# Kernel tuning notes

Measured on AMD Instinct MI355X. Metric: run time of the kernel, lower is better.

## Reference

```python
import math
import jax, jax.numpy as jnp
import numpy as np

HEADS = 8
D = 128            # model_dim
PE = D // 2        # position_embedding_size (query_positional_score=True)
MAXP = 32          # max_position_embeddings
LN_EPS = 1e-5


def setup_inputs() -> dict:
    key = jax.random.key(0)
    ks = jax.random.split(key, 7)
    bs, h, w = 8, 32, 32
    hidden_state = jax.random.normal(ks[0], (bs, h, w, D), dtype=jnp.float32)
    row_emb = jax.random.normal(ks[1], (2 * MAXP - 1, PE), dtype=jnp.float32) * 0.02
    col_emb = jax.random.normal(ks[2], (2 * MAXP - 1, PE), dtype=jnp.float32) * 0.02
    # torch Linear weights are (out_features, in_features)
    Wq = jax.random.normal(ks[3], (HEADS * D, D), dtype=jnp.float32) / math.sqrt(D)
    Wk = jax.random.normal(ks[4], (HEADS * D, D), dtype=jnp.float32) / math.sqrt(D)
    Wv = jax.random.normal(ks[5], (D, HEADS * D), dtype=jnp.float32) / math.sqrt(HEADS * D)
    bv = jnp.zeros((D,), dtype=jnp.float32)
    ln_g = jnp.ones((D,), dtype=jnp.float32)
    ln_b = jnp.zeros((D,), dtype=jnp.float32)
    return {"hidden_state": hidden_state, "row_emb": row_emb, "col_emb": col_emb,
            "Wq": Wq, "Wk": Wk, "Wv": Wv, "bv": bv, "ln_g": ln_g, "ln_b": ln_b}


def _layer_norm(x, g, b):
    mu = jnp.mean(x, axis=-1, keepdims=True)
    var = jnp.var(x, axis=-1, keepdims=True)
    return (x - mu) * jax.lax.rsqrt(var + LN_EPS) * g + b


def _forward(hidden_state, row_emb, col_emb, Wq, Wk, Wv, bv, ln_g, ln_b):
    bs, h, w, _ = hidden_state.shape
    x = _layer_norm(hidden_state, ln_g, ln_b)  # pre_norm=True
    sqrt_norm = math.sqrt(D)

    # relative indices (static, h == w == 32 here)
    deltas = np.arange(MAXP)[None, :] - np.arange(MAXP)[:, None]
    rel = deltas + MAXP - 1
    row_embeds = row_emb[rel[:w, :w]]  # (w, w, PE)
    col_embeds = col_emb[rel[:h, :h]]  # (h, h, PE)

    # projections; original does .view(bs, w, h, heads, D) on a (bs,h,w,heads*D) tensor
    q = jnp.einsum('bhwc,oc->bhwo', x, Wq).reshape(bs, w, h, HEADS, D)
    k = jnp.einsum('bhwc,oc->bhwo', x, Wk).reshape(bs, w, h, HEADS, D)

    q_row = q[..., :PE]
    q_col = q[..., PE:]
    row_scores = jnp.einsum('bijhd,ikd->bijhk', q_row, row_embeds)
    col_scores = jnp.einsum('bijhd,jld->bijhl', q_col, col_embeds)
    scores = (row_scores[..., :, None] + col_scores[..., None, :]) / sqrt_norm  # bijhkl
    scores = scores.transpose(0, 2, 1, 3, 5, 4)

    content = jnp.einsum('bijhd,bklhd->bijhkl', q, k) / sqrt_norm
    scores = scores + content.transpose(0, 2, 1, 3, 5, 4)  # (bs, h, w, heads, h, w)

    attn_shape = scores.shape
    probs = jax.nn.softmax(scores.reshape(*attn_shape[:-2], -1), axis=-1).reshape(attn_shape)

    # dropout omitted (inference / p=0)
    context = jnp.einsum('bijhkl,bkld->bijhd', probs, x)
    context = context.reshape(bs, h, w, HEADS * D)
    output = jnp.einsum('bhwc,oc->bhwo', context, Wv) + bv + x
    return output, probs


def reference(hidden_state, row_emb, col_emb, Wq, Wk, Wv, bv, ln_g, ln_b):
    return _forward(hidden_state, row_emb, col_emb, Wq, Wk, Wv, bv, ln_g, ln_b)
```

## Files before the change

kernel.cpp:

```cpp
#include <hip/hip_runtime.h>
#include <hip/hip_bf16.h>

#define HEADS 8
#define D 128
#define QSCALE 0.12751743f

typedef unsigned short u16;
typedef unsigned int u32;
typedef __attribute__((ext_vector_type(8))) short short8;
typedef __attribute__((ext_vector_type(4))) float f32x4;

static __device__ inline float sbf2f(short s) {
    return __uint_as_float(((u32)(unsigned short)s) << 16);
}
static __device__ inline u16 f2bf(float f) {
    u32 u = __float_as_uint(f);
    return (u16)((u + 0x7FFFu + ((u >> 16) & 1u)) >> 16);
}
static __device__ inline u32 pk2bf(float a, float b) {
    return (u32)f2bf(a) | ((u32)f2bf(b) << 16);
}
static __device__ inline u32 cvtpk(float a, float b) {
    union { __hip_bfloat162 h; u32 u; } x;
    x.h = __float22bfloat162_rn(make_float2(a, b));
    return x.u;
}
static __device__ inline f32x4 mfma16(short8 a, short8 b, f32x4 c) {
    return __builtin_amdgcn_mfma_f32_16x16x32_bf16(a, b, c, 0, 0, 0);
}
static __device__ inline short8 cvt8(const float* e) {
    f32x4 v0 = *(const f32x4*)e;
    f32x4 v1 = *(const f32x4*)(e + 4);
    union { uint4 u; short8 s; } x;
    x.u = make_uint4(pk2bf(v0[0], v0[1]), pk2bf(v0[2], v0[3]),
                     pk2bf(v1[0], v1[1]), pk2bf(v1[2], v1[3]));
    return x.s;
}
static __device__ __forceinline__ void gload_lds16(const void* g, void* l) {
    __builtin_amdgcn_global_load_lds(
        (const __attribute__((address_space(1))) u32*)g,
        (__attribute__((address_space(3))) u32*)(u32)(uintptr_t)l,
        16, 0, 0);
}

__global__ __launch_bounds__(256) void k_init(const float* __restrict__ hs,
    const float* __restrict__ g, const float* __restrict__ bb,
    const float* __restrict__ Wq, const float* __restrict__ Wk,
    const float* __restrict__ Wv,
    float* __restrict__ xf, u16* __restrict__ xbf, u16* __restrict__ xt,
    u16* __restrict__ wqk, u16* __restrict__ wv)
{
    __shared__ __align__(16) u16 tl[128][136];
    int bid = blockIdx.x;
    int tid = threadIdx.x;
    if (bid < 384) {
        int idx = (bid * 256 + tid) * 4;
        const float* src;
        u16* dst;
        if (idx < 131072)      { src = Wq + idx;            dst = wqk + idx; }
        else if (idx < 262144) { src = Wk + (idx - 131072); dst = wqk + idx; }
        else                   { src = Wv + (idx - 262144); dst = wv + (idx - 262144); }
        f32x4 v = *(const f32x4*)src;
        *(uint2*)dst = make_uint2(pk2bf(v[0], v[1]), pk2bf(v[2], v[3]));
        return;
    }
    int blk = bid - 384;
    int b = blk >> 3, ch = blk & 7;
    int c4 = (tid & 31) * 4;
    f32x4 g4 = *(const f32x4*)(g + c4);
    f32x4 b4 = *(const f32x4*)(bb + c4);
    const float* src = hs + ((size_t)b * 1024 + ch * 128) * 128;
    #pragma unroll
    for (int it = 0; it < 16; ++it) {
        int p = (tid >> 5) + it * 8;
        f32x4 v = *(const f32x4*)(src + (size_t)p * 128 + c4);
        float s1 = (v[0] + v[1]) + (v[2] + v[3]);
        float s2 = (v[0] * v[0] + v[1] * v[1]) + (v[2] * v[2] + v[3] * v[3]);
        #pragma unroll
        for (int off = 1; off < 32; off <<= 1) {
            s1 += __shfl_xor(s1, off);
            s2 += __shfl_xor(s2, off);
        }
        float mu  = s1 * 0.0078125f;
        float var = s2 * 0.0078125f - mu * mu;
        float inv = rsqrtf(var + 1e-5f);
        f32x4 o;
        #pragma unroll
        for (int q = 0; q < 4; ++q) o[q] = (v[q] - mu) * inv * g4[q] + b4[q];
        size_t row = (size_t)b * 1024 + ch * 128 + p;
        *(f32x4*)(xf + row * 128 + c4) = o;
        *(uint2*)(xbf + row * 128 + c4) = make_uint2(pk2bf(o[0], o[1]), pk2bf(o[2], o[3]));
        tl[c4 + 0][p] = f2bf(o[0]);
        tl[c4 + 1][p] = f2bf(o[1]);
        tl[c4 + 2][p] = f2bf(o[2]);
        tl[c4 + 3][p] = f2bf(o[3]);
    }
    __syncthreads();
    u16* dst = xt + (size_t)b * 131072 + ch * 128;
    #pragma unroll
    for (int i = 0; i < 8; ++i) {
        int d = (tid >> 4) + i * 16, c8 = (tid & 15) * 8;
        *(uint4*)(dst + (size_t)d * 1024 + c8) = *(const uint4*)&tl[d][c8];
    }
}

__global__ __launch_bounds__(256) void k_proj(const u16* __restrict__ xbf,
    const u16* __restrict__ wqk,
    u16* __restrict__ q_bf, u16* __restrict__ kt_bf)
{
    int tid = threadIdx.x;
    int w = tid >> 6, l = tid & 63, h = l >> 4, ln = l & 15;
    int t0 = blockIdx.x * 64 + w * 16;
    int o0 = blockIdx.y * 64;
    short8 tb[4];
    #pragma unroll
    for (int s = 0; s < 4; ++s)
        tb[s] = *(const short8*)(xbf + (size_t)(t0 + ln) * 128 + s * 32 + h * 8);
    f32x4 acc[4];
    #pragma unroll
    for (int n = 0; n < 4; ++n) acc[n] = f32x4{0.f, 0.f, 0.f, 0.f};
    #pragma unroll
    for (int n = 0; n < 4; ++n) {
        const u16* wsrc = wqk + (size_t)(o0 + n * 16 + ln) * 128;
        #pragma unroll
        for (int s = 0; s < 4; ++s) {
            short8 wf = *(const short8*)(wsrc + s * 32 + h * 8);
            acc[n] = mfma16(wf, tb[s], acc[n]);
        }
    }
    bool isq = (o0 < 1024);
    float os = isq ? QSCALE : 1.0f;
    int head = (o0 & 1023) >> 7;
    int od = (o0 & 127);
    u16* basep = isq ? q_bf : kt_bf;
    int t = t0 + ln;
    int b = t >> 10, pos = t & 1023;
    size_t row;
    if (isq) row = (size_t)(b * 8 + head) * 1024 + pos;
    else { int I = pos >> 5, J = pos & 31; row = (size_t)(b * 8 + head) * 1024 + (J * 32 + I); }
    u16* dst = basep + row * 128 + od + h * 4;
    #pragma unroll
    for (int n = 0; n < 4; ++n) {
        *(uint2*)(dst + n * 16) = make_uint2(
            pk2bf(acc[n][0] * os, acc[n][1] * os),
            pk2bf(acc[n][2] * os, acc[n][3] * os));
    }
}

__global__ __launch_bounds__(256) void k_bias(const u16* __restrict__ q_bf,
    const float* __restrict__ row_emb, const float* __restrict__ col_emb,
    float* __restrict__ rbias, float* __restrict__ cbias)
{
    __shared__ __align__(16) float cbf[32][68];
    int tid = threadIdx.x;
    int w = tid >> 6, l = tid & 63, h = l >> 4, ln = l & 15;
    int blk = blockIdx.x;
    int bh = blk >> 5, I = blk & 31;
    const u16* qb = q_bf + ((size_t)bh * 1024 + I * 32) * 128;
    size_t obase = (size_t)blk * 1024;
    if (w < 2) {
        short8 a0 = *(const short8*)(qb + (size_t)(w * 16 + ln) * 128 + h * 8);
        short8 a1 = *(const short8*)(qb + (size_t)(w * 16 + ln) * 128 + 32 + h * 8);
        f32x4 o[2] = {f32x4{0,0,0,0}, f32x4{0,0,0,0}};
        #pragma unroll
        for (int n = 0; n < 2; ++n) {
            int K = n * 16 + ln;
            const float* e = row_emb + (size_t)(K - I + 31) * 64 + h * 8;
            o[n] = mfma16(a0, cvt8(e), o[n]);
            o[n] = mfma16(a1, cvt8(e + 32), o[n]);
        }
        #pragma unroll
        for (int n = 0; n < 2; ++n)
            #pragma unroll
            for (int r = 0; r < 4; ++r)
                rbias[obase + (size_t)(w * 16 + h * 4 + r) * 32 + n * 16 + ln] = o[n][r];
    } else {
        int m = w - 2;
        short8 a0 = *(const short8*)(qb + (size_t)(m * 16 + ln) * 128 + 64 + h * 8);
        short8 a1 = *(const short8*)(qb + (size_t)(m * 16 + ln) * 128 + 96 + h * 8);
        f32x4 o[4] = {f32x4{0,0,0,0}, f32x4{0,0,0,0}, f32x4{0,0,0,0}, f32x4{0,0,0,0}};
        #pragma unroll
        for (int n = 0; n < 4; ++n) {
            int p = n * 16 + ln;
            if (p > 62) p = 62;
            const float* e = col_emb + (size_t)p * 64 + h * 8;
            o[n] = mfma16(a0, cvt8(e), o[n]);
            o[n] = mfma16(a1, cvt8(e + 32), o[n]);
        }
        #pragma unroll
        for (int n = 0; n < 4; ++n)
            #pragma unroll
            for (int r = 0; r < 4; ++r)
                cbf[m * 16 + h * 4 + r][n * 16 + ln] = o[n][r];
    }
    __syncthreads();
    int J = tid >> 3, L0 = (tid & 7) * 4;
    float4 g;
    g.x = cbf[J][L0 + 0 - J + 31];
    g.y = cbf[J][L0 + 1 - J + 31];
    g.z = cbf[J][L0 + 2 - J + 31];
    g.w = cbf[J][L0 + 3 - J + 31];
    *(float4*)(cbias + obase + (size_t)J * 32 + L0) = g;
}

__global__ __launch_bounds__(512, 4) void k_attn(const u16* __restrict__ q_bf,
    const u16* __restrict__ kt_bf, const u16* __restrict__ xt_bf,
    const float* __restrict__ rbias, const float* __restrict__ cbias,
    float* __restrict__ probs, u16* __restrict__ ctx_bf)
{
    __shared__ __align__(16) char KT[8 * 8192];
    __shared__ float wred[256];

    int tid = threadIdx.x;
    int w = tid >> 6, l = tid & 63, h = l >> 4, ln = l & 15;
    int flat = blockIdx.x;
    int bh = flat >> 5, I = flat & 31;
    int b = bh >> 3, head = bh & 7;
    int kk0 = w * 128;
    char* reg = KT + w * 8192;
    const char* ktg = (const char*)(kt_bf + ((size_t)bh * 1024 + kk0) * 128);
    int d0 = w * 16;
    const u16* xb = xt_bf + (size_t)b * 131072 + (size_t)(d0 + ln) * 1024 + h * 8;

    const float* rbase = rbias + (size_t)(bh * 32 + I) * 1024;
    const float* cbase = cbias + (size_t)(bh * 32 + I) * 1024;
    f32x4 rbr[2][2], cbr[2];
    #pragma unroll
    for (int n = 0; n < 2; ++n) {
        int J = n * 16 + ln;
        rbr[n][0] = *(const f32x4*)(rbase + J * 32 + h * 4);
        rbr[n][1] = *(const f32x4*)(rbase + J * 32 + 16 + h * 4);
        cbr[n]    = *(const f32x4*)(cbase + J * 32 + w * 4);
    }
    const u16* qbase = q_bf + ((size_t)bh * 1024 + I * 32) * 128;
    short8 q0[4], q1[4];
    #pragma unroll
    for (int s = 0; s < 4; ++s) {
        q0[s] = *(const short8*)(qbase + (size_t)ln * 128 + s * 32 + h * 8);
        q1[s] = *(const short8*)(qbase + (size_t)(16 + ln) * 128 + s * 32 + h * 8);
    }

    auto stage_chunk = [&](int c, int buf) {
        const char* gs = ktg + c * 4096;
        char* ld = reg + buf * 4096;
        #pragma unroll
        for (int i = 0; i < 4; ++i) {
            int key = ((i * 4 + (l >> 4)) & 7) << 4;
            int o = i * 1024 + l * 16;
            gload_lds16(gs + (o ^ key), ld + i * 1024);
        }
    };
    stage_chunk(0, 0);
    stage_chunk(1, 1);

    f32x4 acc[2][8];
    #pragma unroll
    for (int n = 0; n < 2; ++n)
        #pragma unroll
        for (int t = 0; t < 8; ++t) acc[n][t] = f32x4{0.f, 0.f, 0.f, 0.f};
    int xk = (ln & 7) << 4;
    #pragma unroll
    for (int c = 0; c < 8; ++c) {
        if (c < 7) asm volatile("s_waitcnt vmcnt(4)" ::: "memory");
        else       asm volatile("s_waitcnt vmcnt(0)" ::: "memory");
        const char* cb = reg + (c & 1) * 4096;
        short8 kf[4];
        #pragma unroll
        for (int s = 0; s < 4; ++s)
            kf[s] = *(const short8*)(cb + ((ln * 256 + s * 64 + h * 16) ^ xk));
        asm volatile("s_waitcnt lgkmcnt(0)" ::: "memory");
        __builtin_amdgcn_sched_barrier(0);
        if (c + 2 < 8) stage_chunk(c + 2, c & 1);
        __builtin_amdgcn_s_setprio(1);
        #pragma unroll
        for (int s = 0; s < 4; ++s) {
            acc[0][c] = mfma16(kf[s], q0[s], acc[0][c]);
            acc[1][c] = mfma16(kf[s], q1[s], acc[1][c]);
        }
        __builtin_amdgcn_s_setprio(0);
    }

    #pragma unroll
    for (int n = 0; n < 2; ++n) {
        int J = n * 16 + ln;
        float sum = 0.f;
        #pragma unroll
        for (int t = 0; t < 8; ++t) {
            float cbv = cbr[n][t >> 1];
            float p0 = exp2f(acc[n][t][0] + rbr[n][t & 1][0] + cbv);
            float p1 = exp2f(acc[n][t][1] + rbr[n][t & 1][1] + cbv);
            float p2 = exp2f(acc[n][t][2] + rbr[n][t & 1][2] + cbv);
            float p3 = exp2f(acc[n][t][3] + rbr[n][t & 1][3] + cbv);
            sum += (p0 + p1) + (p2 + p3);
            *(uint2*)(reg + ((J * 256 + t * 32 + h * 8) ^ xk)) =
                make_uint2(cvtpk(p0, p1), cvtpk(p2, p3));
        }
        sum += __shfl_xor(sum, 16);
        sum += __shfl_xor(sum, 32);
        if (l < 16) wred[w * 32 + J] = sum;
    }
    __syncthreads();

    f32x4 sum0 = f32x4{0.f, 0.f, 0.f, 0.f};
    f32x4 sum1 = f32x4{0.f, 0.f, 0.f, 0.f};
    #pragma unroll
    for (int w2 = 0; w2 < 8; ++w2) {
        sum0 += *(const f32x4*)&wred[w2 * 32 + h * 4];
        sum1 += *(const f32x4*)&wred[w2 * 32 + 16 + h * 4];
    }
    int j = tid >> 4;
    float sd = 0.f;
    #pragma unroll
    for (int w2 = 0; w2 < 8; ++w2) sd += wred[w2 * 32 + j];
    float invd = 1.0f / sd;

    f32x4 cacc[2] = {f32x4{0,0,0,0}, f32x4{0,0,0,0}};
    __builtin_amdgcn_s_setprio(1);
    #pragma unroll
    for (int ks = 0; ks < 32; ++ks) {
        short8 xf8 = *(const short8*)(xb + ks * 32);
        #pragma unroll
        for (int m = 0; m < 2; ++m) {
            short8 pa = *(const short8*)(KT + (ks >> 2) * 8192 +
                (((m * 16 + ln) * 256 + (ks & 3) * 64 + h * 16) ^ xk));
            cacc[m] = mfma16(pa, xf8, cacc[m]);
        }
    }
    __builtin_amdgcn_s_setprio(0);
    #pragma unroll
    for (int m = 0; m < 2; ++m)
        #pragma unroll
        for (int r = 0; r < 4; ++r) {
            int J = m * 16 + h * 4 + r;
            float inv = 1.0f / (m ? sum1[r] : sum0[r]);
            ctx_bf[((size_t)(b * 32 + J) * 32 + I) * 1024 + head * 128 + d0 + ln] =
                f2bf(cacc[m][r] * inv);
        }

    {
        float* prow = probs + ((((size_t)(b * 32 + j) * 32 + I) * 8 + head) << 10);
        int jx = (j & 7) << 4;
        #pragma unroll
        for (int i = 0; i < 8; ++i) {
            int kk = i * 128 + (tid & 15) * 8;
            short8 pv = *(const short8*)(KT + i * 8192 +
                            ((j * 256 + (tid & 15) * 16) ^ jx));
            float4 o0, o1;
            o0.x = sbf2f(pv[0]) * invd; o0.y = sbf2f(pv[1]) * invd;
            o0.z = sbf2f(pv[2]) * invd; o0.w = sbf2f(pv[3]) * invd;
            o1.x = sbf2f(pv[4]) * invd; o1.y = sbf2f(pv[5]) * invd;
            o1.z = sbf2f(pv[6]) * invd; o1.w = sbf2f(pv[7]) * invd;
            *(float4*)(prow + kk)     = o0;
            *(float4*)(prow + kk + 4) = o1;
        }
    }
}

__global__ __launch_bounds__(256) void k_out(const u16* __restrict__ ctx_bf,
    const u16* __restrict__ wv_bf, const float* __restrict__ bv,
    const float* __restrict__ xf, float* __restrict__ out)
{
    int tid = threadIdx.x;
    int w = tid >> 6, l = tid & 63, h = l >> 4, ln = l & 15;
    int wm = w >> 1, wn = w & 1;
    int t0 = blockIdx.x * 32 + wm * 16;
    int o0 = blockIdx.y * 64 + wn * 32;
    f32x4 acc[2] = {f32x4{0,0,0,0}, f32x4{0,0,0,0}};
    for (int ks = 0; ks < 32; ++ks) {
        short8 a = *(const short8*)(ctx_bf + (size_t)(t0 + ln) * 1024 + ks * 32 + h * 8);
        #pragma unroll
        for (int nt = 0; nt < 2; ++nt) {
            short8 bb = *(const short8*)(wv_bf + (size_t)(o0 + nt * 16 + ln) * 1024 + ks * 32 + h * 8);
            acc[nt] = mfma16(a, bb, acc[nt]);
        }
    }
    #pragma unroll
    for (int nt = 0; nt < 2; ++nt) {
        int o = o0 + nt * 16 + ln;
        float bvv = bv[o];
        #pragma unroll
        for (int r = 0; r < 4; ++r) {
            int t = t0 + h * 4 + r;
            out[(size_t)t * 128 + o] = acc[nt][r] + bvv + xf[(size_t)t * 128 + o];
        }
    }
}

extern "C" void kernel_launch(void* const* d_in, const int* in_sizes, int n_in,
                              void* d_out, int out_size, void* d_ws, size_t ws_size,
                              hipStream_t stream) {
    (void)in_sizes; (void)n_in; (void)out_size; (void)ws_size;
    const float* hs      = (const float*)d_in[0];
    const float* row_emb = (const float*)d_in[1];
    const float* col_emb = (const float*)d_in[2];
    const float* Wq      = (const float*)d_in[3];
    const float* Wk      = (const float*)d_in[4];
    const float* Wv      = (const float*)d_in[5];
    const float* bv      = (const float*)d_in[6];
    const float* ln_g    = (const float*)d_in[7];
    const float* ln_b    = (const float*)d_in[8];

    float* out   = (float*)d_out;
    float* probs = out + 1048576;

    char* ws = (char*)d_ws;
    float* xf     = (float*)(ws);
    u16*   xbf    = (u16*)(ws + 4194304);
    u16*   q_bf   = (u16*)(ws + 6291456);
    u16*   kt_bf  = (u16*)(ws + 23068672);
    u16*   xt     = (u16*)(ws + 39845888);
    u16*   wqk_bf = (u16*)(ws + 41943040);
    u16*   wv_bf  = (u16*)(ws + 42467328);
    u16*   ctx    = (u16*)(ws + 42729472);
    float* rbias  = (float*)(ws + 59506688);
    float* cbias  = (float*)(ws + 67895296);

    k_init <<<448, 256, 0, stream>>>(hs, ln_g, ln_b, Wq, Wk, Wv,
                                     xf, xbf, xt, wqk_bf, wv_bf);
    k_proj <<<dim3(128, 32), 256, 0, stream>>>(xbf, wqk_bf, q_bf, kt_bf);
    k_bias <<<2048, 256, 0, stream>>>(q_bf, row_emb, col_emb, rbias, cbias);
    k_attn <<<2048, 512, 0, stream>>>(q_bf, kt_bf, xt, rbias, cbias, probs, ctx);
    k_out  <<<dim3(256, 2), 256, 0, stream>>>(ctx, wv_bf, bv, xf, out);
}
```

Baseline: 250.2 us.

## Fuse row-bias computation into attention kernel and drop setprio hints

The row positional bias is now computed inside the attention kernel with MFMA against the query fragments already held in registers, instead of being written to and read back from a global rbias buffer. The separate bias kernel now computes only the column bias, spreading that work over all four waves. This removes the rbias global round-trip (about 8 MB written and read). In exchange the attention kernel does extra MFMAs and row_emb loads per block, which may raise register pressure. The s_setprio hints around the MFMA loops are also removed.

Result: no change. 249.5 us (-0.3%).

```diff
diff --git a/kernel.cpp b/kernel.cpp
--- a/kernel.cpp
+++ b/kernel.cpp
@@ -147,9 +147,8 @@
     }
 }
 
-__global__ __launch_bounds__(256) void k_bias(const u16* __restrict__ q_bf,
-    const float* __restrict__ row_emb, const float* __restrict__ col_emb,
-    float* __restrict__ rbias, float* __restrict__ cbias)
+__global__ __launch_bounds__(256) void k_cbias(const u16* __restrict__ q_bf,
+    const float* __restrict__ col_emb, float* __restrict__ cbias)
 {
     __shared__ __align__(16) float cbf[32][68];
     int tid = threadIdx.x;
@@ -158,54 +157,37 @@
     int bh = blk >> 5, I = blk & 31;
     const u16* qb = q_bf + ((size_t)bh * 1024 + I * 32) * 128;
     size_t obase = (size_t)blk * 1024;
-    if (w < 2) {
-        short8 a0 = *(const short8*)(qb + (size_t)(w * 16 + ln) * 128 + h * 8);
-        short8 a1 = *(const short8*)(qb + (size_t)(w * 16 + ln) * 128 + 32 + h * 8);
-        f32x4 o[2] = {f32x4{0,0,0,0}, f32x4{0,0,0,0}};
-        #pragma unroll
-        for (int n = 0; n < 2; ++n) {
-            int K = n * 16 + ln;
-            const float* e = row_emb + (size_t)(K - I + 31) * 64 + h * 8;
-            o[n] = mfma16(a0, cvt8(e), o[n]);
-            o[n] = mfma16(a1, cvt8(e + 32), o[n]);
-        }
-        #pragma unroll
-        for (int n = 0; n < 2; ++n)
-            #pragma unroll
-            for (int r = 0; r < 4; ++r)
-                rbias[obase + (size_t)(w * 16 + h * 4 + r) * 32 + n * 16 + ln] = o[n][r];
-    } else {
-        int m = w - 2;
-        short8 a0 = *(const short8*)(qb + (size_t)(m * 16 + ln) * 128 + 64 + h * 8);
-        short8 a1 = *(const short8*)(qb + (size_t)(m * 16 + ln) * 128 + 96 + h * 8);
-        f32x4 o[4] = {f32x4{0,0,0,0}, f32x4{0,0,0,0}, f32x4{0,0,0,0}, f32x4{0,0,0,0}};
-        #pragma unroll
-        for (int n = 0; n < 4; ++n) {
-            int p = n * 16 + ln;
-            if (p > 62) p = 62;
-            const float* e = col_emb + (size_t)p * 64 + h * 8;
-            o[n] = mfma16(a0, cvt8(e), o[n]);
-            o[n] = mfma16(a1, cvt8(e + 32), o[n]);
-        }
-        #pragma unroll
-        for (int n = 0; n < 4; ++n)
-            #pragma unroll
-            for (int r = 0; r < 4; ++r)
-                cbf[m * 16 + h * 4 + r][n * 16 + ln] = o[n][r];
-    }
+    int m  = w & 1;
+    int np = (w >> 1) * 2;
+    short8 a0 = *(const short8*)(qb + (size_t)(m * 16 + ln) * 128 + 64 + h * 8);
+    short8 a1 = *(const short8*)(qb + (size_t)(m * 16 + ln) * 128 + 96 + h * 8);
+    f32x4 o[2] = {f32x4{0,0,0,0}, f32x4{0,0,0,0}};
+    #pragma unroll
+    for (int ni = 0; ni < 2; ++ni) {
+        int p = (np + ni) * 16 + ln;
+        if (p > 62) p = 62;
+        const float* e = col_emb + (size_t)p * 64 + h * 8;
+        o[ni] = mfma16(a0, cvt8(e), o[ni]);
+        o[ni] = mfma16(a1, cvt8(e + 32), o[ni]);
+    }
+    #pragma unroll
+    for (int ni = 0; ni < 2; ++ni)
+        #pragma unroll
+        for (int r = 0; r < 4; ++r)
+            cbf[m * 16 + h * 4 + r][(np + ni) * 16 + ln] = o[ni][r];
     __syncthreads();
     int J = tid >> 3, L0 = (tid & 7) * 4;
-    float4 g;
-    g.x = cbf[J][L0 + 0 - J + 31];
-    g.y = cbf[J][L0 + 1 - J + 31];
-    g.z = cbf[J][L0 + 2 - J + 31];
-    g.w = cbf[J][L0 + 3 - J + 31];
-    *(float4*)(cbias + obase + (size_t)J * 32 + L0) = g;
+    float4 gg;
+    gg.x = cbf[J][L0 + 0 - J + 31];
+    gg.y = cbf[J][L0 + 1 - J + 31];
+    gg.z = cbf[J][L0 + 2 - J + 31];
+    gg.w = cbf[J][L0 + 3 - J + 31];
+    *(float4*)(cbias + obase + (size_t)J * 32 + L0) = gg;
 }
 
 __global__ __launch_bounds__(512, 4) void k_attn(const u16* __restrict__ q_bf,
     const u16* __restrict__ kt_bf, const u16* __restrict__ xt_bf,
-    const float* __restrict__ rbias, const float* __restrict__ cbias,
+    const float* __restrict__ row_emb, const float* __restrict__ cbias,
     float* __restrict__ probs, u16* __restrict__ ctx_bf)
 {
     __shared__ __align__(16) char KT[8 * 8192];
@@ -222,16 +204,11 @@
     int d0 = w * 16;
     const u16* xb = xt_bf + (size_t)b * 131072 + (size_t)(d0 + ln) * 1024 + h * 8;
 
-    const float* rbase = rbias + (size_t)(bh * 32 + I) * 1024;
     const float* cbase = cbias + (size_t)(bh * 32 + I) * 1024;
-    f32x4 rbr[2][2], cbr[2];
-    #pragma unroll
-    for (int n = 0; n < 2; ++n) {
-        int J = n * 16 + ln;
-        rbr[n][0] = *(const f32x4*)(rbase + J * 32 + h * 4);
-        rbr[n][1] = *(const f32x4*)(rbase + J * 32 + 16 + h * 4);
-        cbr[n]    = *(const f32x4*)(cbase + J * 32 + w * 4);
-    }
+    f32x4 cbr[2];
+    #pragma unroll
+    for (int n = 0; n < 2; ++n)
+        cbr[n] = *(const f32x4*)(cbase + (n * 16 + ln) * 32 + w * 4);
     const u16* qbase = q_bf + ((size_t)bh * 1024 + I * 32) * 128;
     short8 q0[4], q1[4];
     #pragma unroll
@@ -252,6 +229,22 @@
     };
     stage_chunk(0, 0);
     stage_chunk(1, 1);
+
+    f32x4 rbr[2][2];
+    #pragma unroll
+    for (int n = 0; n < 2; ++n)
+        #pragma unroll
+        for (int par = 0; par < 2; ++par) rbr[n][par] = f32x4{0.f, 0.f, 0.f, 0.f};
+    #pragma unroll
+    for (int par = 0; par < 2; ++par) {
+        #pragma unroll
+        for (int s = 0; s < 2; ++s) {
+            short8 re = cvt8(row_emb + (size_t)(par * 16 + ln - I + 31) * 64
+                                     + s * 32 + h * 8);
+            rbr[0][par] = mfma16(re, q0[s], rbr[0][par]);
+            rbr[1][par] = mfma16(re, q1[s], rbr[1][par]);
+        }
+    }
 
     f32x4 acc[2][8];
     #pragma unroll
@@ -271,13 +264,11 @@
         asm volatile("s_waitcnt lgkmcnt(0)" ::: "memory");
         __builtin_amdgcn_sched_barrier(0);
         if (c + 2 < 8) stage_chunk(c + 2, c & 1);
-        __builtin_amdgcn_s_setprio(1);
         #pragma unroll
         for (int s = 0; s < 4; ++s) {
             acc[0][c] = mfma16(kf[s], q0[s], acc[0][c]);
             acc[1][c] = mfma16(kf[s], q1[s], acc[1][c]);
         }
-        __builtin_amdgcn_s_setprio(0);
     }
 
     #pragma unroll
@@ -315,7 +306,6 @@
     float invd = 1.0f / sd;
 
     f32x4 cacc[2] = {f32x4{0,0,0,0}, f32x4{0,0,0,0}};
-    __builtin_amdgcn_s_setprio(1);
     #pragma unroll
     for (int ks = 0; ks < 32; ++ks) {
         short8 xf8 = *(const short8*)(xb + ks * 32);
@@ -326,7 +316,6 @@
             cacc[m] = mfma16(pa, xf8, cacc[m]);
         }
     }
-    __builtin_amdgcn_s_setprio(0);
     #pragma unroll
     for (int m = 0; m < 2; ++m)
         #pragma unroll
@@ -412,13 +401,12 @@
     u16*   wqk_bf = (u16*)(ws + 41943040);
     u16*   wv_bf  = (u16*)(ws + 42467328);
     u16*   ctx    = (u16*)(ws + 42729472);
-    float* rbias  = (float*)(ws + 59506688);
-    float* cbias  = (float*)(ws + 67895296);
-
-    k_init <<<448, 256, 0, stream>>>(hs, ln_g, ln_b, Wq, Wk, Wv,
-                                     xf, xbf, xt, wqk_bf, wv_bf);
-    k_proj <<<dim3(128, 32), 256, 0, stream>>>(xbf, wqk_bf, q_bf, kt_bf);
-    k_bias <<<2048, 256, 0, stream>>>(q_bf, row_emb, col_emb, rbias, cbias);
-    k_attn <<<2048, 512, 0, stream>>>(q_bf, kt_bf, xt, rbias, cbias, probs, ctx);
-    k_out  <<<dim3(256, 2), 256, 0, stream>>>(ctx, wv_bf, bv, xf, out);
-}
+    float* cbias  = (float*)(ws + 59506688);
+
+    k_init  <<<448, 256, 0, stream>>>(hs, ln_g, ln_b, Wq, Wk, Wv,
+                                      xf, xbf, xt, wqk_bf, wv_bf);
+    k_proj  <<<dim3(128, 32), 256, 0, stream>>>(xbf, wqk_bf, q_bf, kt_bf);
+    k_cbias <<<2048, 256, 0, stream>>>(q_bf, col_emb, cbias);
+    k_attn  <<<2048, 512, 0, stream>>>(q_bf, kt_bf, xt, row_emb, cbias, probs, ctx);
+    k_out   <<<dim3(256, 2), 256, 0, stream>>>(ctx, wv_bf, bv, xf, out);
+}
```
